# Optimization experiments

Hardware: AMD Instinct MI355X
Metric: run time of the kernel (lower is better)

The kernel has to match this reference:

```python
import jax, jax.numpy as jnp
import numpy as np
import math

IN_DIM = 512
LR_MUL = 1.0
SCALE = (1.0 / math.sqrt(IN_DIM)) * LR_MUL  # EqualLinear runtime weight scale


def setup_inputs() -> dict:
    key = jax.random.key(0)
    k1, k2 = jax.random.split(key)
    x = jax.random.normal(k1, (256, 18, 18, 512), dtype=jnp.float32)  # [B, n_out, n_layers, in_dim]
    W = jax.random.normal(k2, (18, 512, 512), dtype=jnp.float32)      # [n_out, out_dim, in_dim]
    b = jnp.zeros((18, 512), dtype=jnp.float32)                        # [n_out, out_dim], bias_init=0
    idx = jnp.arange(18, dtype=jnp.int32)                              # n_indx
    return {"x": x, "W": W, "b": b, "idx": idx}


def reference(x, W, b, idx):
    # Fused equivalent of the nested loops: for each direction i, apply
    # EqualLinear_i to slices x[:, i, j, :] for j in idx, writing results back.
    x_sel = x[:, :, idx, :]                                    # [B, O, J, D_in]
    y = jnp.einsum('koji,odi->kojd', x_sel, W) * SCALE         # [B, O, J, D_out]
    y = y + (b * LR_MUL)[None, :, None, :]
    return x.at[:, :, idx, :].set(y)
```

## Files before the change

### kernel.cpp

```cpp
#include <hip/hip_runtime.h>
#include <hip/hip_bf16.h>


typedef __bf16  bf16x8  __attribute__((ext_vector_type(8)));
typedef float   floatx4 __attribute__((ext_vector_type(4)));

#define O_DIM 18
#define J_DIM 18
#define KB    256
#define C_DIM 512
#define BM    128
#define BN    128
#define BK    32
#define NK    (C_DIM / BK)
#define LDSS  40

__device__ __forceinline__ __bf16 f2bf(float f) { return (__bf16)f; }

__device__ __forceinline__ void barrier_lds() {
    asm volatile("" ::: "memory");
    __builtin_amdgcn_s_waitcnt(0xc07f);
    __builtin_amdgcn_s_barrier();
    asm volatile("" ::: "memory");
}

__global__ __launch_bounds__(256, 2)
void dirnet_gemm(const float* __restrict__ x, const float* __restrict__ W,
                 const float* __restrict__ bias, const int* __restrict__ idx,
                 float* __restrict__ out)
{
    const int id  = blockIdx.x;
    const int xcd = id & 7;
    const int r   = id >> 3;
    const int nt  = r & 3;
    const int q   = r >> 2;
    const int T   = xcd * 81 + q;
    const int o   = T / 36;
    const int rem = T - o * 36;
    const int j   = rem >> 1;
    const int mt  = rem & 1;
    const int jj  = idx[j];

    __shared__ __bf16 As[BM * LDSS];
    __shared__ __bf16 Bs[BN * LDSS];

    const int tid  = threadIdx.x;
    const int srow = tid >> 2;
    const int scol = (tid & 3) << 3;

    const float* xp = x + ((size_t)((mt * BM + srow) * O_DIM + o) * J_DIM + jj) * C_DIM + scol;
    const size_t xRS = (size_t)64 * O_DIM * J_DIM * C_DIM;
    const float* wp = W + ((size_t)(o * C_DIM + nt * BN + srow)) * C_DIM + scol;
    const size_t wRS = (size_t)64 * C_DIM;

    const int lane = tid & 63;
    const int wv   = tid >> 6;
    const int mOff = (wv & 1) * 64;
    const int nOff = (wv >> 1) * 64;
    const int lrow = lane & 15;
    const int lk   = (lane >> 4) << 3;

    floatx4 acc[4][4] = {};
    float4 pa[2][2][2];
    float4 pb[2][2][2];

#define LOAD_A(set, kk)                                                \
    {                                                                  \
        _Pragma("unroll")                                              \
        for (int p = 0; p < 2; ++p) {                                  \
            pa[set][p][0] = *(const float4*)(xp + p * xRS + (kk));     \
            pa[set][p][1] = *(const float4*)(xp + p * xRS + (kk) + 4); \
        }                                                              \
    }
#define LOAD_B(set, kk)                                                \
    {                                                                  \
        _Pragma("unroll")                                              \
        for (int p = 0; p < 2; ++p) {                                  \
            pb[set][p][0] = *(const float4*)(wp + p * wRS + (kk));     \
            pb[set][p][1] = *(const float4*)(wp + p * wRS + (kk) + 4); \
        }                                                              \
    }
#define CVT_AB(set, sa, sb)                                                   \
    {                                                                         \
        _Pragma("unroll")                                                     \
        for (int p = 0; p < 2; ++p) {                                         \
            sa[p][0]=f2bf(pa[set][p][0].x); sa[p][1]=f2bf(pa[set][p][0].y);   \
            sa[p][2]=f2bf(pa[set][p][0].z); sa[p][3]=f2bf(pa[set][p][0].w);   \
            sa[p][4]=f2bf(pa[set][p][1].x); sa[p][5]=f2bf(pa[set][p][1].y);   \
            sa[p][6]=f2bf(pa[set][p][1].z); sa[p][7]=f2bf(pa[set][p][1].w);   \
        }                                                                     \
        _Pragma("unroll")                                                     \
        for (int p = 0; p < 2; ++p) {                                         \
            sb[p][0]=f2bf(pb[set][p][0].x); sb[p][1]=f2bf(pb[set][p][0].y);   \
            sb[p][2]=f2bf(pb[set][p][0].z); sb[p][3]=f2bf(pb[set][p][0].w);   \
            sb[p][4]=f2bf(pb[set][p][1].x); sb[p][5]=f2bf(pb[set][p][1].y);   \
            sb[p][6]=f2bf(pb[set][p][1].z); sb[p][7]=f2bf(pb[set][p][1].w);   \
        }                                                                     \
    }
#define STORE_AB(sa, sb)                                               \
    {                                                                  \
        _Pragma("unroll")                                              \
        for (int p = 0; p < 2; ++p) {                                  \
            *(bf16x8*)&As[(p * 64 + srow) * LDSS + scol] = sa[p];      \
            *(bf16x8*)&Bs[(p * 64 + srow) * LDSS + scol] = sb[p];      \
        }                                                              \
    }

    LOAD_A(0, 0);       LOAD_B(0, 0);
    LOAD_A(1, BK);      LOAD_B(1, BK);

    #pragma unroll
    for (int t = 0; t < NK; ++t) {
        const int s = t & 1;

        bf16x8 sa[2], sb[2];
        CVT_AB(s, sa, sb);

        barrier_lds();
        STORE_AB(sa, sb);
        barrier_lds();

        if (t + 2 < NK) {
            const int k2 = (t + 2) * BK;
            LOAD_A(s, k2);
            LOAD_B(s, k2);
        }

        bf16x8 af[4], bfr[4];
        #pragma unroll
        for (int mi = 0; mi < 4; ++mi)
            af[mi] = *(const bf16x8*)&As[(mOff + mi * 16 + lrow) * LDSS + lk];
        #pragma unroll
        for (int ni = 0; ni < 4; ++ni)
            bfr[ni] = *(const bf16x8*)&Bs[(nOff + ni * 16 + lrow) * LDSS + lk];

        #pragma unroll
        for (int mi = 0; mi < 4; ++mi)
            #pragma unroll
            for (int ni = 0; ni < 4; ++ni)
                acc[mi][ni] = __builtin_amdgcn_mfma_f32_16x16x32_bf16(
                    af[mi], bfr[ni], acc[mi][ni], 0, 0, 0);
    }

#undef LOAD_A
#undef LOAD_B
#undef CVT_AB
#undef STORE_AB

    const float scale = 0.04419417382415922f;
    const int rbase = (lane >> 4) << 2;
    #pragma unroll
    for (int ni = 0; ni < 4; ++ni) {
        const int d  = nt * BN + nOff + ni * 16 + lrow;
        const float bv = bias[o * C_DIM + d];
        #pragma unroll
        for (int mi = 0; mi < 4; ++mi) {
            #pragma unroll
            for (int r2 = 0; r2 < 4; ++r2) {
                const int kr = mt * BM + mOff + mi * 16 + rbase + r2;
                out[((size_t)(kr * O_DIM + o) * J_DIM + jj) * C_DIM + d] =
                    acc[mi][ni][r2] * scale + bv;
            }
        }
    }
}

__global__ void copy_nonsel(const float* __restrict__ x, const int* __restrict__ idx,
                            float* __restrict__ out)
{
    const int jj = blockIdx.x;
    const int o  = blockIdx.y;
    bool member = false;
    for (int t = 0; t < J_DIM; ++t) member = member || (idx[t] == jj);
    if (member) return;
    const int tid = threadIdx.x;
    for (int k = 0; k < KB; ++k) {
        const size_t base = ((size_t)(k * O_DIM + o) * J_DIM + jj) * C_DIM;
        for (int c = tid * 4; c < C_DIM; c += 256 * 4) {
            *(float4*)&out[base + c] = *(const float4*)&x[base + c];
        }
    }
}

extern "C" void kernel_launch(void* const* d_in, const int* in_sizes, int n_in,
                              void* d_out, int out_size, void* d_ws, size_t ws_size,
                              hipStream_t stream) {
    const float* x   = (const float*)d_in[0];
    const float* W   = (const float*)d_in[1];
    const float* b   = (const float*)d_in[2];
    const int*   idx = (const int*)d_in[3];
    float* out = (float*)d_out;

    dirnet_gemm<<<dim3(2 * 4 * J_DIM * O_DIM), 256, 0, stream>>>(x, W, b, idx, out);
    copy_nonsel<<<dim3(J_DIM, O_DIM), 256, 0, stream>>>(x, idx, out);
}
```

Before: 374.3 us.

## Enlarge GEMM tile to 256x256 with 512-thread blocks

```diff
diff --git a/kernel.cpp b/kernel.cpp
--- a/kernel.cpp
+++ b/kernel.cpp
@@ -9,8 +9,8 @@
 #define J_DIM 18
 #define KB    256
 #define C_DIM 512
-#define BM    128
-#define BN    128
+#define BM    256
+#define BN    256
 #define BK    32
 #define NK    (C_DIM / BK)
 #define LDSS  40
@@ -24,118 +24,98 @@
     asm volatile("" ::: "memory");
 }
 
-__global__ __launch_bounds__(256, 2)
+__global__ __launch_bounds__(512, 2)
 void dirnet_gemm(const float* __restrict__ x, const float* __restrict__ W,
                  const float* __restrict__ bias, const int* __restrict__ idx,
                  float* __restrict__ out)
 {
     const int id  = blockIdx.x;
     const int xcd = id & 7;
-    const int r   = id >> 3;
-    const int nt  = r & 3;
-    const int q   = r >> 2;
+    const int q   = id >> 3;
     const int T   = xcd * 81 + q;
     const int o   = T / 36;
     const int rem = T - o * 36;
     const int j   = rem >> 1;
-    const int mt  = rem & 1;
+    const int nt  = rem & 1;
     const int jj  = idx[j];
 
     __shared__ __bf16 As[BM * LDSS];
     __shared__ __bf16 Bs[BN * LDSS];
 
     const int tid  = threadIdx.x;
-    const int srow = tid >> 2;
-    const int scol = (tid & 3) << 3;
+    const int srow = tid >> 1;
+    const int scol = (tid & 1) << 4;
 
-    const float* xp = x + ((size_t)((mt * BM + srow) * O_DIM + o) * J_DIM + jj) * C_DIM + scol;
-    const size_t xRS = (size_t)64 * O_DIM * J_DIM * C_DIM;
+    const float* xp = x + ((size_t)(srow * O_DIM + o) * J_DIM + jj) * C_DIM + scol;
     const float* wp = W + ((size_t)(o * C_DIM + nt * BN + srow)) * C_DIM + scol;
-    const size_t wRS = (size_t)64 * C_DIM;
 
     const int lane = tid & 63;
     const int wv   = tid >> 6;
-    const int mOff = (wv & 1) * 64;
+    const int mOff = (wv & 1) * 128;
     const int nOff = (wv >> 1) * 64;
     const int lrow = lane & 15;
     const int lk   = (lane >> 4) << 3;
 
-    floatx4 acc[4][4] = {};
-    float4 pa[2][2][2];
-    float4 pb[2][2][2];
+    floatx4 acc[8][4] = {};
+    float4 pa[2][4];
+    float4 pb[4];
 
-#define LOAD_A(set, kk)                                                \
-    {                                                                  \
-        _Pragma("unroll")                                              \
-        for (int p = 0; p < 2; ++p) {                                  \
-            pa[set][p][0] = *(const float4*)(xp + p * xRS + (kk));     \
-            pa[set][p][1] = *(const float4*)(xp + p * xRS + (kk) + 4); \
-        }                                                              \
+#define LOAD_A(set, kk)                                          \
+    {                                                            \
+        _Pragma("unroll")                                        \
+        for (int v = 0; v < 4; ++v)                              \
+            pa[set][v] = *(const float4*)(xp + (kk) + v * 4);    \
     }
-#define LOAD_B(set, kk)                                                \
-    {                                                                  \
-        _Pragma("unroll")                                              \
-        for (int p = 0; p < 2; ++p) {                                  \
-            pb[set][p][0] = *(const float4*)(wp + p * wRS + (kk));     \
-            pb[set][p][1] = *(const float4*)(wp + p * wRS + (kk) + 4); \
-        }                                                              \
+#define LOAD_B(kk)                                               \
+    {                                                            \
+        _Pragma("unroll")                                        \
+        for (int v = 0; v < 4; ++v)                              \
+            pb[v] = *(const float4*)(wp + (kk) + v * 4);         \
     }
-#define CVT_AB(set, sa, sb)                                                   \
+#define CVT4(pv, s0, s1)                                                      \
     {                                                                         \
-        _Pragma("unroll")                                                     \
-        for (int p = 0; p < 2; ++p) {                                         \
-            sa[p][0]=f2bf(pa[set][p][0].x); sa[p][1]=f2bf(pa[set][p][0].y);   \
-            sa[p][2]=f2bf(pa[set][p][0].z); sa[p][3]=f2bf(pa[set][p][0].w);   \
-            sa[p][4]=f2bf(pa[set][p][1].x); sa[p][5]=f2bf(pa[set][p][1].y);   \
-            sa[p][6]=f2bf(pa[set][p][1].z); sa[p][7]=f2bf(pa[set][p][1].w);   \
-        }                                                                     \
-        _Pragma("unroll")                                                     \
-        for (int p = 0; p < 2; ++p) {                                         \
-            sb[p][0]=f2bf(pb[set][p][0].x); sb[p][1]=f2bf(pb[set][p][0].y);   \
-            sb[p][2]=f2bf(pb[set][p][0].z); sb[p][3]=f2bf(pb[set][p][0].w);   \
-            sb[p][4]=f2bf(pb[set][p][1].x); sb[p][5]=f2bf(pb[set][p][1].y);   \
-            sb[p][6]=f2bf(pb[set][p][1].z); sb[p][7]=f2bf(pb[set][p][1].w);   \
-        }                                                                     \
-    }
-#define STORE_AB(sa, sb)                                               \
-    {                                                                  \
-        _Pragma("unroll")                                              \
-        for (int p = 0; p < 2; ++p) {                                  \
-            *(bf16x8*)&As[(p * 64 + srow) * LDSS + scol] = sa[p];      \
-            *(bf16x8*)&Bs[(p * 64 + srow) * LDSS + scol] = sb[p];      \
-        }                                                              \
+        s0[0]=f2bf(pv[0].x); s0[1]=f2bf(pv[0].y);                             \
+        s0[2]=f2bf(pv[0].z); s0[3]=f2bf(pv[0].w);                             \
+        s0[4]=f2bf(pv[1].x); s0[5]=f2bf(pv[1].y);                             \
+        s0[6]=f2bf(pv[1].z); s0[7]=f2bf(pv[1].w);                             \
+        s1[0]=f2bf(pv[2].x); s1[1]=f2bf(pv[2].y);                             \
+        s1[2]=f2bf(pv[2].z); s1[3]=f2bf(pv[2].w);                             \
+        s1[4]=f2bf(pv[3].x); s1[5]=f2bf(pv[3].y);                             \
+        s1[6]=f2bf(pv[3].z); s1[7]=f2bf(pv[3].w);                             \
     }
 
-    LOAD_A(0, 0);       LOAD_B(0, 0);
-    LOAD_A(1, BK);      LOAD_B(1, BK);
+    LOAD_A(0, 0);
+    LOAD_B(0);
+    LOAD_A(1, BK);
 
     #pragma unroll
     for (int t = 0; t < NK; ++t) {
         const int s = t & 1;
 
-        bf16x8 sa[2], sb[2];
-        CVT_AB(s, sa, sb);
+        bf16x8 sa0, sa1, sb0, sb1;
+        CVT4(pa[s], sa0, sa1);
+        CVT4(pb,    sb0, sb1);
 
         barrier_lds();
-        STORE_AB(sa, sb);
+        *(bf16x8*)&As[srow * LDSS + scol]     = sa0;
+        *(bf16x8*)&As[srow * LDSS + scol + 8] = sa1;
+        *(bf16x8*)&Bs[srow * LDSS + scol]     = sb0;
+        *(bf16x8*)&Bs[srow * LDSS + scol + 8] = sb1;
         barrier_lds();
 
-        if (t + 2 < NK) {
-            const int k2 = (t + 2) * BK;
-            LOAD_A(s, k2);
-            LOAD_B(s, k2);
-        }
+        if (t + 1 < NK) LOAD_B((t + 1) * BK);
+        if (t + 2 < NK) LOAD_A(s, (t + 2) * BK);
 
-        bf16x8 af[4], bfr[4];
+        bf16x8 af[8], bfr[4];
         #pragma unroll
-        for (int mi = 0; mi < 4; ++mi)
+        for (int mi = 0; mi < 8; ++mi)
             af[mi] = *(const bf16x8*)&As[(mOff + mi * 16 + lrow) * LDSS + lk];
         #pragma unroll
         for (int ni = 0; ni < 4; ++ni)
             bfr[ni] = *(const bf16x8*)&Bs[(nOff + ni * 16 + lrow) * LDSS + lk];
 
         #pragma unroll
-        for (int mi = 0; mi < 4; ++mi)
+        for (int mi = 0; mi < 8; ++mi)
             #pragma unroll
             for (int ni = 0; ni < 4; ++ni)
                 acc[mi][ni] = __builtin_amdgcn_mfma_f32_16x16x32_bf16(
@@ -144,8 +124,7 @@
 
 #undef LOAD_A
 #undef LOAD_B
-#undef CVT_AB
-#undef STORE_AB
+#undef CVT4
 
     const float scale = 0.04419417382415922f;
     const int rbase = (lane >> 4) << 2;
@@ -154,10 +133,10 @@
         const int d  = nt * BN + nOff + ni * 16 + lrow;
         const float bv = bias[o * C_DIM + d];
         #pragma unroll
-        for (int mi = 0; mi < 4; ++mi) {
+        for (int mi = 0; mi < 8; ++mi) {
             #pragma unroll
             for (int r2 = 0; r2 < 4; ++r2) {
-                const int kr = mt * BM + mOff + mi * 16 + rbase + r2;
+                const int kr = mOff + mi * 16 + rbase + r2;
                 out[((size_t)(kr * O_DIM + o) * J_DIM + jj) * C_DIM + d] =
                     acc[mi][ni][r2] * scale + bv;
             }
@@ -191,6 +170,6 @@
     const int*   idx = (const int*)d_in[3];
     float* out = (float*)d_out;
 
-    dirnet_gemm<<<dim3(2 * 4 * J_DIM * O_DIM), 256, 0, stream>>>(x, W, b, idx, out);
+    dirnet_gemm<<<dim3(2 * J_DIM * O_DIM), 512, 0, stream>>>(x, W, b, idx, out);
     copy_nonsel<<<dim3(J_DIM, O_DIM), 256, 0, stream>>>(x, idx, out);
 }
```

After: 371.3 us. About the same (-0.8%).
